# Kernel optimization log

Hardware: AMD Instinct MI355X
Metric: run time of the kernel (lower is better)

Reference implementation:

```python
import jax, jax.numpy as jnp
import numpy as np

N, IN_DIM, HID, H1, NCLS, H2, E = 50000, 256, 32, 8, 16, 8, 800000


def gat_conv(x, edge_index, W, a_src, a_dst, b, H, C):
    """PyG-style GATConv, eval mode (attention dropout off), concat=True,
    negative_slope=0.2, add_self_loops=True."""
    n = x.shape[0]
    loop = jnp.arange(n)
    src = jnp.concatenate([edge_index[0], loop])  # [E+N]
    dst = jnp.concatenate([edge_index[1], loop])
    h = (x @ W).reshape(n, H, C)                  # [N,H,C]
    alpha_s = jnp.sum(h * a_src, axis=-1)         # [N,H]
    alpha_d = jnp.sum(h * a_dst, axis=-1)         # [N,H]
    e = jax.nn.leaky_relu(alpha_s[src] + alpha_d[dst], 0.2)  # [E+N,H]
    # segment softmax over incoming edges of each target node
    e_max = jax.ops.segment_max(e, dst, num_segments=n)      # [N,H] (self-loop guarantees nonempty)
    p = jnp.exp(e - e_max[dst])
    denom = jax.ops.segment_sum(p, dst, num_segments=n)
    alpha = p / (denom[dst] + 1e-16)              # [E+N,H]
    msg = h[src] * alpha[:, :, None]              # [E+N,H,C]
    out = jax.ops.segment_sum(msg, dst, num_segments=n)      # [N,H,C]
    return out.reshape(n, H * C) + b


def setup_inputs() -> dict:
    key = jax.random.key(0)
    ks = jax.random.split(key, 12)
    x = jax.random.normal(ks[0], (N, IN_DIM), dtype=jnp.float32)
    edge_index = jax.random.randint(ks[1], (2, E), 0, N, dtype=jnp.int64)
    s1 = 1.0 / np.sqrt(IN_DIM)
    s2 = 1.0 / np.sqrt(HID * H1)
    W1 = jax.random.normal(ks[2], (IN_DIM, H1 * HID), dtype=jnp.float32) * s1
    a_src1 = jax.random.normal(ks[3], (H1, HID), dtype=jnp.float32) * s1
    a_dst1 = jax.random.normal(ks[4], (H1, HID), dtype=jnp.float32) * s1
    b1 = jnp.zeros((H1 * HID,), dtype=jnp.float32)
    W2 = jax.random.normal(ks[5], (H1 * HID, H2 * NCLS), dtype=jnp.float32) * s2
    a_src2 = jax.random.normal(ks[6], (H2, NCLS), dtype=jnp.float32) * s2
    a_dst2 = jax.random.normal(ks[7], (H2, NCLS), dtype=jnp.float32) * s2
    b2 = jnp.zeros((H2 * NCLS,), dtype=jnp.float32)
    return {"x": x, "edge_index": edge_index, "W1": W1, "a_src1": a_src1,
            "a_dst1": a_dst1, "b1": b1, "W2": W2, "a_src2": a_src2,
            "a_dst2": a_dst2, "b2": b2}


def reference(x, edge_index, W1, a_src1, a_dst1, b1, W2, a_src2, a_dst2, b2):
    # eval mode: F.dropout is identity
    h = gat_conv(x, edge_index, W1, a_src1, a_dst1, b1, H1, HID)   # [N, H1*HID]
    h = jax.nn.elu(h)
    h = gat_conv(h, edge_index, W2, a_src2, a_dst2, b2, H2, NCLS)  # [N, H2*NCLS]
    return jax.nn.log_softmax(h, axis=1)
```

## Files before the change

### kernel.cpp

```cpp
#include <hip/hip_runtime.h>
#include <hip/hip_fp16.h>

#define NN 50000
#define NE 800000

typedef _Float16 half4v __attribute__((ext_vector_type(4)));
typedef _Float16 half8v __attribute__((ext_vector_type(8)));
typedef float f32x4 __attribute__((ext_vector_type(4)));

#define Q_SCALE 0.04724409448f
#define Q_INV   21.16666667f

static __device__ __forceinline__ float lrelu(float x) { return x > 0.f ? x : 0.2f * x; }

__global__ void detect_i64_kernel(const unsigned* __restrict__ ei, int* __restrict__ flag) {
  if (threadIdx.x == 0 && blockIdx.x == 0) {
    int is64 = 1;
    for (int i = 0; i < 64; ++i)
      if (ei[2 * i + 1] != 0u) { is64 = 0; break; }
    *flag = is64;
  }
}

static __device__ __forceinline__ int edge_at(const void* ei, int is64, long long idx) {
  if (is64) return (int)((const long long*)ei)[idx];
  return ((const int*)ei)[idx];
}

__global__ void count_kernel(const void* __restrict__ ei, const int* __restrict__ flag,
                             int* __restrict__ counts) {
  int e = blockIdx.x * blockDim.x + threadIdx.x;
  if (e >= NE) return;
  int is64 = *flag;
  int d = edge_at(ei, is64, (long long)NE + e);
  atomicAdd(&counts[d], 1);
}

static __device__ __forceinline__ int block_scan_inc(int v, int tid) {
  __shared__ int ws[4];
  const int lane = tid & 63, wv = tid >> 6;
  #pragma unroll
  for (int off = 1; off < 64; off <<= 1) {
    int t = __shfl_up(v, off);
    if (lane >= off) v += t;
  }
  if (lane == 63) ws[wv] = v;
  __syncthreads();
  int add = 0;
  #pragma unroll
  for (int j = 0; j < 4; ++j) if (j < wv) add += ws[j];
  return v + add;
}

__global__ void scan1_kernel(const int* __restrict__ counts, int* __restrict__ bsums) {
  __shared__ int ws[4];
  const int tid = threadIdx.x;
  const int lane = tid & 63, wv = tid >> 6;
  int i = blockIdx.x * 256 + tid;
  int v = (i < NN) ? counts[i] : 0;
  #pragma unroll
  for (int off = 1; off < 64; off <<= 1) v += __shfl_xor(v, off);
  if (lane == 0) ws[wv] = v;
  __syncthreads();
  if (tid == 0) bsums[blockIdx.x] = ws[0] + ws[1] + ws[2] + ws[3];
}

__global__ void scan2_kernel(int* __restrict__ bsums, int nb) {
  const int tid = threadIdx.x;
  int v = (tid < nb) ? bsums[tid] : 0;
  int inc = block_scan_inc(v, tid);
  if (tid < nb) bsums[tid] = inc - v;
}

__global__ void scan3_kernel(const int* __restrict__ counts, const int* __restrict__ bsums,
                             int* __restrict__ rs) {
  const int tid = threadIdx.x;
  int i = blockIdx.x * 256 + tid;
  int v = (i < NN) ? counts[i] : 0;
  int inc = block_scan_inc(v, tid);
  if (i < NN) rs[i + 1] = bsums[blockIdx.x] + inc;
  if (i == 0) rs[0] = 0;
}

__global__ void scatter_kernel(const void* __restrict__ ei, const int* __restrict__ flag,
                               const int* __restrict__ rs, int* __restrict__ cursor,
                               int* __restrict__ ssrc) {
  int e = blockIdx.x * blockDim.x + threadIdx.x;
  if (e >= NE) return;
  int is64 = *flag;
  int s = edge_at(ei, is64, e);
  int d = edge_at(ei, is64, (long long)NE + e);
  int p = atomicAdd(&cursor[d], 1);
  ssrc[rs[d] + p] = s;
}

__global__ void prep_kernel(const float* __restrict__ W1, const float* __restrict__ W2,
                            const float* __restrict__ aS1, const float* __restrict__ aD1,
                            const float* __restrict__ aS2, const float* __restrict__ aD2,
                            _Float16* __restrict__ W1p, _Float16* __restrict__ W2p,
                            _Float16* __restrict__ Wa1p, _Float16* __restrict__ Wa2p) {
  int i = blockIdx.x * blockDim.x + threadIdx.x;
  if (i < 65536) {
    int j = i & 7, l = (i >> 3) & 63, kst = (i >> 9) & 7, ct = i >> 12;
    int col = ct * 16 + (l & 15);
    int k = kst * 32 + ((l >> 4) << 3) + j;
    W1p[i] = (_Float16)W1[(size_t)k * 256 + col];
  } else if (i < 98304) {
    int n = i - 65536;
    int j = n & 7, l = (n >> 3) & 63, kst = (n >> 9) & 7, ct = n >> 12;
    int col = ct * 16 + (l & 15);
    int k = kst * 32 + ((l >> 4) << 3) + j;
    W2p[n] = (_Float16)W2[(size_t)k * 128 + col];
  } else if (i < 102400) {
    int n = i - 98304;
    int j = n & 7, l = (n >> 3) & 63, kst = n >> 9;
    int row = l & 15;
    int head = row & 7;
    const float* a = (row < 8) ? aS1 : aD1;
    int k = kst * 32 + ((l >> 4) << 3) + j;
    float s = 0.f;
    #pragma unroll 8
    for (int c = 0; c < 32; ++c)
      s += W1[(size_t)k * 256 + head * 32 + c] * a[head * 32 + c];
    Wa1p[n] = (_Float16)s;
  } else if (i < 106496) {
    int n = i - 102400;
    int j = n & 7, l = (n >> 3) & 63, kst = n >> 9;
    int row = l & 15;
    int head = row & 7;
    const float* a = (row < 8) ? aS2 : aD2;
    int k = kst * 32 + ((l >> 4) << 3) + j;
    float s = 0.f;
    #pragma unroll 8
    for (int c = 0; c < 16; ++c)
      s += W2[(size_t)k * 128 + head * 16 + c] * a[head * 16 + c];
    Wa2p[n] = (_Float16)s;
  }
}

template<int BN, int NCF, bool A_HALF, bool Q8OUT>
__global__ __launch_bounds__(512) void gemm_mfma(const void* __restrict__ Araw,
                                                 const _Float16* __restrict__ Bp,
                                                 const _Float16* __restrict__ Wap,
                                                 void* __restrict__ Cout,
                                                 float* __restrict__ alS,
                                                 float* __restrict__ alD, int M) {
  __shared__ __align__(16) _Float16 As[64][256 + 8];
  const int tid = threadIdx.x;
  const int bm0 = blockIdx.x * 64;
  if (A_HALF) {
    const _Float16* A = (const _Float16*)Araw;
    half8v tmp[4]; int rr[4], cc[4];
    #pragma unroll
    for (int t = 0; t < 4; ++t) {
      int idx = tid + t * 512;
      int r = idx >> 5, c8 = (idx & 31) << 3;
      int gr = bm0 + r;
      tmp[t] = (half8v){};
      if (gr < M) tmp[t] = *(const half8v*)&A[(size_t)gr * 256 + c8];
      rr[t] = r; cc[t] = c8;
    }
    #pragma unroll
    for (int t = 0; t < 4; ++t)
      *(half8v*)&As[rr[t]][cc[t]] = tmp[t];
  } else {
    const float* A = (const float*)Araw;
    #pragma unroll
    for (int g = 0; g < 2; ++g) {
      float4 tmp[4]; int rr[4], cc[4];
      #pragma unroll
      for (int t = 0; t < 4; ++t) {
        int idx = tid + (g * 4 + t) * 512;
        int r = idx >> 6, c4 = (idx & 63) << 2;
        int gr = bm0 + r;
        tmp[t] = make_float4(0.f, 0.f, 0.f, 0.f);
        if (gr < M) tmp[t] = *(const float4*)&A[(size_t)gr * 256 + c4];
        rr[t] = r; cc[t] = c4;
      }
      #pragma unroll
      for (int t = 0; t < 4; ++t) {
        half4v h = { (_Float16)tmp[t].x, (_Float16)tmp[t].y,
                     (_Float16)tmp[t].z, (_Float16)tmp[t].w };
        *(half4v*)&As[rr[t]][cc[t]] = h;
      }
    }
  }
  __syncthreads();
  const int lane = tid & 63, wv = tid >> 6;
  const int ncol0 = wv * (16 * NCF);
  const int lrow = lane & 15, lk8 = (lane >> 4) << 3;
  f32x4 acc[4][NCF];
  f32x4 acca[4];
  #pragma unroll
  for (int rf = 0; rf < 4; ++rf) {
    acca[rf] = (f32x4){0.f, 0.f, 0.f, 0.f};
    #pragma unroll
    for (int cf = 0; cf < NCF; ++cf) acc[rf][cf] = (f32x4){0.f, 0.f, 0.f, 0.f};
  }
  #pragma unroll
  for (int kst = 0; kst < 8; ++kst) {
    const int ks = kst * 32 + lk8;
    half8v af[4];
    #pragma unroll
    for (int rf = 0; rf < 4; ++rf)
      af[rf] = *(const half8v*)&As[16 * rf + lrow][ks];
    #pragma unroll
    for (int cf = 0; cf < NCF; ++cf) {
      half8v bf = *(const half8v*)&Bp[((size_t)((wv * NCF + cf) * 8 + kst) * 64 + lane) * 8];
      #pragma unroll
      for (int rf = 0; rf < 4; ++rf)
        acc[rf][cf] = __builtin_amdgcn_mfma_f32_16x16x32_f16(af[rf], bf, acc[rf][cf], 0, 0, 0);
    }
    if (wv == 0) {
      half8v bfa = *(const half8v*)&Wap[((size_t)kst * 64 + lane) * 8];
      #pragma unroll
      for (int rf = 0; rf < 4; ++rf)
        acca[rf] = __builtin_amdgcn_mfma_f32_16x16x32_f16(af[rf], bfa, acca[rf], 0, 0, 0);
    }
  }
  if (Q8OUT) {
    __syncthreads();
    char* Cs = (char*)&As[0][0];
    #pragma unroll
    for (int rf = 0; rf < 4; ++rf) {
      #pragma unroll
      for (int j = 0; j < 4; ++j) {
        int r = 16 * rf + 4 * ((lane >> 4) & 3) + j;
        #pragma unroll
        for (int cf = 0; cf < NCF; ++cf) {
          int col = ncol0 + 16 * cf + lrow;
          float v = acc[rf][cf][j];
          int q = __float2int_rn(fminf(fmaxf(v * Q_INV, -127.f), 127.f)) + 128;
          Cs[r * 272 + col] = (char)q;
        }
      }
    }
    __syncthreads();
    unsigned char* C8 = (unsigned char*)Cout;
    #pragma unroll
    for (int g = 0; g < 2; ++g) {
      int idx = tid + g * 512;
      int r = idx >> 4, c16 = idx & 15;
      int grow = bm0 + r;
      if (grow < M)
        *(int4*)&C8[(size_t)grow * 256 + 16 * c16] = *(const int4*)&Cs[r * 272 + 16 * c16];
    }
  } else {
    __half* C = (__half*)Cout;
    #pragma unroll
    for (int rf = 0; rf < 4; ++rf) {
      #pragma unroll
      for (int j = 0; j < 4; ++j) {
        int row = bm0 + 16 * rf + 4 * ((lane >> 4) & 3) + j;
        if (row < M) {
          #pragma unroll
          for (int cf = 0; cf < NCF; ++cf) {
            int col = ncol0 + 16 * cf + lrow;
            C[(size_t)row * BN + col] = __float2half(acc[rf][cf][j]);
          }
        }
      }
    }
  }
  if (wv == 0) {
    #pragma unroll
    for (int rf = 0; rf < 4; ++rf) {
      #pragma unroll
      for (int j = 0; j < 4; ++j) {
        int row = bm0 + 16 * rf + 4 * ((lane >> 4) & 3) + j;
        if (row < M) {
          float v = acca[rf][j];
          if (lrow < 8) alS[row * 8 + lrow] = v;
          else          alD[row * 8 + (lrow - 8)] = v;
        }
      }
    }
  }
}

#define ACCQ(w, p) do { \
    ax0 += (p) * (float)((w) & 255u); \
    ax1 += (p) * (float)(((w) >> 8) & 255u); \
    ax2 += (p) * (float)(((w) >> 16) & 255u); \
    ax3 += (p) * (float)((w) >> 24); \
  } while (0)

__global__ __launch_bounds__(256) void agg1_kernel(const unsigned char* __restrict__ h1q,
    const float* __restrict__ as, const float* __restrict__ ad,
    const int* __restrict__ rs, const int* __restrict__ ssrc,
    const float* __restrict__ bias, __half* __restrict__ out) {
  const int wid = (blockIdx.x * blockDim.x + threadIdx.x) >> 6;
  const int lane = threadIdx.x & 63;
  if (wid >= NN) return;
  const int node = wid;
  const int beg = rs[node], end = rs[node + 1];
  const int deg = end - beg;
  const int hd = lane >> 3;
  const float advh = ad[node * 8 + hd];
  const unsigned* hw = (const unsigned*)h1q;
  float denom = 0.f;
  float ax0 = 0.f, ax1 = 0.f, ax2 = 0.f, ax3 = 0.f;
  {
    float p = __expf(lrelu(as[node * 8 + hd] + advh));
    unsigned w = hw[(size_t)node * 64 + lane];
    ACCQ(w, p);
    denom = p;
  }
  for (int base = 0; base < deg; base += 64) {
    const int cnt = min(deg - base, 64);
    int sv = (lane < cnt) ? ssrc[beg + base + lane] : 0;
    int j = 0;
    for (; j + 8 <= cnt; j += 8) {
      int s0 = __builtin_amdgcn_readlane(sv, j + 0);
      int s1 = __builtin_amdgcn_readlane(sv, j + 1);
      int s2 = __builtin_amdgcn_readlane(sv, j + 2);
      int s3 = __builtin_amdgcn_readlane(sv, j + 3);
      int s4 = __builtin_amdgcn_readlane(sv, j + 4);
      int s5 = __builtin_amdgcn_readlane(sv, j + 5);
      int s6 = __builtin_amdgcn_readlane(sv, j + 6);
      int s7 = __builtin_amdgcn_readlane(sv, j + 7);
      float b0 = as[s0 * 8 + hd], b1 = as[s1 * 8 + hd];
      float b2 = as[s2 * 8 + hd], b3 = as[s3 * 8 + hd];
      float b4 = as[s4 * 8 + hd], b5 = as[s5 * 8 + hd];
      float b6 = as[s6 * 8 + hd], b7 = as[s7 * 8 + hd];
      unsigned w0 = hw[(size_t)s0 * 64 + lane];
      unsigned w1 = hw[(size_t)s1 * 64 + lane];
      unsigned w2 = hw[(size_t)s2 * 64 + lane];
      unsigned w3 = hw[(size_t)s3 * 64 + lane];
      unsigned w4 = hw[(size_t)s4 * 64 + lane];
      unsigned w5 = hw[(size_t)s5 * 64 + lane];
      unsigned w6 = hw[(size_t)s6 * 64 + lane];
      unsigned w7 = hw[(size_t)s7 * 64 + lane];
      float p0 = __expf(lrelu(b0 + advh)), p1 = __expf(lrelu(b1 + advh));
      float p2 = __expf(lrelu(b2 + advh)), p3 = __expf(lrelu(b3 + advh));
      float p4 = __expf(lrelu(b4 + advh)), p5 = __expf(lrelu(b5 + advh));
      float p6 = __expf(lrelu(b6 + advh)), p7 = __expf(lrelu(b7 + advh));
      denom += (p0 + p1) + (p2 + p3) + ((p4 + p5) + (p6 + p7));
      ACCQ(w0, p0); ACCQ(w1, p1); ACCQ(w2, p2); ACCQ(w3, p3);
      ACCQ(w4, p4); ACCQ(w5, p5); ACCQ(w6, p6); ACCQ(w7, p7);
    }
    for (; j < cnt; ++j) {
      int s = __builtin_amdgcn_readlane(sv, j);
      float p = __expf(lrelu(as[s * 8 + hd] + advh));
      unsigned w = hw[(size_t)s * 64 + lane];
      ACCQ(w, p);
      denom += p;
    }
  }
  const float inv = 1.f / (denom + 1e-16f);
  const float4 bv = *(const float4*)&bias[lane * 4];
  float4 o;
  o.x = Q_SCALE * (ax0 * inv - 128.f) + bv.x;
  o.y = Q_SCALE * (ax1 * inv - 128.f) + bv.y;
  o.z = Q_SCALE * (ax2 * inv - 128.f) + bv.z;
  o.w = Q_SCALE * (ax3 * inv - 128.f) + bv.w;
  o.x = o.x > 0.f ? o.x : __expf(o.x) - 1.f;
  o.y = o.y > 0.f ? o.y : __expf(o.y) - 1.f;
  o.z = o.z > 0.f ? o.z : __expf(o.z) - 1.f;
  o.w = o.w > 0.f ? o.w : __expf(o.w) - 1.f;
  union { __half2 h2[2]; float2 f2; } w;
  w.h2[0] = __floats2half2_rn(o.x, o.y);
  w.h2[1] = __floats2half2_rn(o.z, o.w);
  *(float2*)&out[(size_t)node * 256 + lane * 4] = w.f2;
}

__global__ __launch_bounds__(256) void agg2_kernel(const __half* __restrict__ h,
    const float* __restrict__ as, const float* __restrict__ ad,
    const int* __restrict__ rs, const int* __restrict__ ssrc,
    const float* __restrict__ bias, float* __restrict__ out) {
  const int wid = (blockIdx.x * blockDim.x + threadIdx.x) >> 6;
  const int lane = threadIdx.x & 63;
  if (wid >= NN) return;
  const int node = wid;
  const int beg = rs[node], end = rs[node + 1];
  const int deg = end - beg;
  const int hd = lane >> 3;
  const float advh = ad[node * 8 + hd];
  float denom;
  __half2 acc;
  {
    float p = __expf(lrelu(as[node * 8 + hd] + advh));
    __half2 q = ((const __half2*)&h[(size_t)node * 128])[lane];
    acc = __hmul2(__float2half2_rn(p), q);
    denom = p;
  }
  for (int base = 0; base < deg; base += 64) {
    const int cnt = min(deg - base, 64);
    int sv = (lane < cnt) ? ssrc[beg + base + lane] : 0;
    int j = 0;
    for (; j + 8 <= cnt; j += 8) {
      int s0 = __builtin_amdgcn_readlane(sv, j + 0);
      int s1 = __builtin_amdgcn_readlane(sv, j + 1);
      int s2 = __builtin_amdgcn_readlane(sv, j + 2);
      int s3 = __builtin_amdgcn_readlane(sv, j + 3);
      int s4 = __builtin_amdgcn_readlane(sv, j + 4);
      int s5 = __builtin_amdgcn_readlane(sv, j + 5);
      int s6 = __builtin_amdgcn_readlane(sv, j + 6);
      int s7 = __builtin_amdgcn_readlane(sv, j + 7);
      float b0 = as[s0 * 8 + hd], b1 = as[s1 * 8 + hd];
      float b2 = as[s2 * 8 + hd], b3 = as[s3 * 8 + hd];
      float b4 = as[s4 * 8 + hd], b5 = as[s5 * 8 + hd];
      float b6 = as[s6 * 8 + hd], b7 = as[s7 * 8 + hd];
      __half2 q0 = ((const __half2*)&h[(size_t)s0 * 128])[lane];
      __half2 q1 = ((const __half2*)&h[(size_t)s1 * 128])[lane];
      __half2 q2 = ((const __half2*)&h[(size_t)s2 * 128])[lane];
      __half2 q3 = ((const __half2*)&h[(size_t)s3 * 128])[lane];
      __half2 q4 = ((const __half2*)&h[(size_t)s4 * 128])[lane];
      __half2 q5 = ((const __half2*)&h[(size_t)s5 * 128])[lane];
      __half2 q6 = ((const __half2*)&h[(size_t)s6 * 128])[lane];
      __half2 q7 = ((const __half2*)&h[(size_t)s7 * 128])[lane];
      float p0 = __expf(lrelu(b0 + advh)), p1 = __expf(lrelu(b1 + advh));
      float p2 = __expf(lrelu(b2 + advh)), p3 = __expf(lrelu(b3 + advh));
      float p4 = __expf(lrelu(b4 + advh)), p5 = __expf(lrelu(b5 + advh));
      float p6 = __expf(lrelu(b6 + advh)), p7 = __expf(lrelu(b7 + advh));
      denom += (p0 + p1) + (p2 + p3) + ((p4 + p5) + (p6 + p7));
      acc = __hfma2(__float2half2_rn(p0), q0, acc);
      acc = __hfma2(__float2half2_rn(p1), q1, acc);
      acc = __hfma2(__float2half2_rn(p2), q2, acc);
      acc = __hfma2(__float2half2_rn(p3), q3, acc);
      acc = __hfma2(__float2half2_rn(p4), q4, acc);
      acc = __hfma2(__float2half2_rn(p5), q5, acc);
      acc = __hfma2(__float2half2_rn(p6), q6, acc);
      acc = __hfma2(__float2half2_rn(p7), q7, acc);
    }
    for (; j < cnt; ++j) {
      int s = __builtin_amdgcn_readlane(sv, j);
      float p = __expf(lrelu(as[s * 8 + hd] + advh));
      __half2 q = ((const __half2*)&h[(size_t)s * 128])[lane];
      acc = __hfma2(__float2half2_rn(p), q, acc);
      denom += p;
    }
  }
  const float inv = 1.f / (denom + 1e-16f);
  float2 av = __half22float2(acc);
  float v0 = av.x * inv + bias[lane * 2 + 0];
  float v1 = av.y * inv + bias[lane * 2 + 1];
  float mx = fmaxf(v0, v1);
  #pragma unroll
  for (int off = 1; off < 64; off <<= 1) mx = fmaxf(mx, __shfl_xor(mx, off));
  float sum = __expf(v0 - mx) + __expf(v1 - mx);
  #pragma unroll
  for (int off = 1; off < 64; off <<= 1) sum += __shfl_xor(sum, off);
  float lse = mx + __logf(sum);
  float2 o = make_float2(v0 - lse, v1 - lse);
  __builtin_nontemporal_store(o.x, &out[(size_t)node * 128 + lane * 2]);
  __builtin_nontemporal_store(o.y, &out[(size_t)node * 128 + lane * 2 + 1]);
}

extern "C" void kernel_launch(void* const* d_in, const int* in_sizes, int n_in,
                              void* d_out, int out_size, void* d_ws, size_t ws_size,
                              hipStream_t stream) {
  const float* x    = (const float*)d_in[0];
  const void*  ei   = d_in[1];
  const float* W1   = (const float*)d_in[2];
  const float* aS1  = (const float*)d_in[3];
  const float* aD1  = (const float*)d_in[4];
  const float* b1   = (const float*)d_in[5];
  const float* W2   = (const float*)d_in[6];
  const float* aS2  = (const float*)d_in[7];
  const float* aD2  = (const float*)d_in[8];
  const float* b2   = (const float*)d_in[9];
  float* out = (float*)d_out;

  char* ws = (char*)d_ws;
  unsigned char* h1q = (unsigned char*)ws; ws += (size_t)NN * 256;
  __half* h2   = (__half*)ws;          ws += (size_t)NN * 128 * 2;
  __half* hmid = (__half*)ws;          ws += (size_t)NN * 256 * 2;
  _Float16* W1p = (_Float16*)ws;       ws += (size_t)65536 * 2;
  _Float16* W2p = (_Float16*)ws;       ws += (size_t)32768 * 2;
  _Float16* Wa1p = (_Float16*)ws;      ws += (size_t)4096 * 2;
  _Float16* Wa2p = (_Float16*)ws;      ws += (size_t)4096 * 2;
  float* alS  = (float*)ws;            ws += (size_t)NN * 8 * 4;
  float* alD  = (float*)ws;            ws += (size_t)NN * 8 * 4;
  int* counts = (int*)ws;              ws += (size_t)NN * 4;
  int* rs     = (int*)ws;              ws += (size_t)(NN + 1) * 4;
  int* bsums  = (int*)ws;              ws += (size_t)256 * 4;
  int* ssrc   = (int*)ws;              ws += (size_t)NE * 4;
  int* flag   = (int*)ws;              ws += 256;

  const int NB = (NN + 255) / 256;

  detect_i64_kernel<<<1, 64, 0, stream>>>((const unsigned*)ei, flag);
  hipMemsetAsync(counts, 0, (size_t)NN * 4, stream);
  count_kernel<<<(NE + 255) / 256, 256, 0, stream>>>(ei, flag, counts);
  scan1_kernel<<<NB, 256, 0, stream>>>(counts, bsums);
  scan2_kernel<<<1, 256, 0, stream>>>(bsums, NB);
  scan3_kernel<<<NB, 256, 0, stream>>>(counts, bsums, rs);
  hipMemsetAsync(counts, 0, (size_t)NN * 4, stream);
  scatter_kernel<<<(NE + 255) / 256, 256, 0, stream>>>(ei, flag, rs, counts, ssrc);

  prep_kernel<<<(106496 + 255) / 256, 256, 0, stream>>>(W1, W2, aS1, aD1, aS2, aD2,
                                                        W1p, W2p, Wa1p, Wa2p);

  const int ngrid = (NN + 63) / 64;
  gemm_mfma<256, 2, false, true><<<ngrid, 512, 0, stream>>>(x, W1p, Wa1p, h1q, alS, alD, NN);
  agg1_kernel<<<(NN + 3) / 4, 256, 0, stream>>>(h1q, alS, alD, rs, ssrc, b1, hmid);

  gemm_mfma<128, 1, true, false><<<ngrid, 512, 0, stream>>>(hmid, W2p, Wa2p, h2, alS, alD, NN);
  agg2_kernel<<<(NN + 3) / 4, 256, 0, stream>>>(h2, alS, alD, rs, ssrc, b2, out);
}
```

Measured before the change: 220.8 us.

## Quantize layer-2 features to uint8 and share attention exps via lane shuffles

The second GEMM now writes its projected features as 8-bit quantized bytes, using the same fixed scale as layer 1. agg2 gathers 2-byte words instead of half2 values and dequantizes into fp32 accumulators, which halves the gather traffic. Both aggregation kernels now compute each neighbor's attention exponent once per lane group and broadcast it with shuffles, instead of every lane loading alpha_src and computing exp. The cost is quantization error in the layer-2 features with a fixed scale that may clip, plus extra shuffle instructions.

```diff
diff --git a/kernel.cpp b/kernel.cpp
--- a/kernel.cpp
+++ b/kernel.cpp
@@ -220,6 +220,7 @@
   }
   if (Q8OUT) {
     __syncthreads();
+    constexpr int ROWB = BN + 16;
     char* Cs = (char*)&As[0][0];
     #pragma unroll
     for (int rf = 0; rf < 4; ++rf) {
@@ -231,19 +232,17 @@
           int col = ncol0 + 16 * cf + lrow;
           float v = acc[rf][cf][j];
           int q = __float2int_rn(fminf(fmaxf(v * Q_INV, -127.f), 127.f)) + 128;
-          Cs[r * 272 + col] = (char)q;
+          Cs[r * ROWB + col] = (char)q;
         }
       }
     }
     __syncthreads();
     unsigned char* C8 = (unsigned char*)Cout;
-    #pragma unroll
-    for (int g = 0; g < 2; ++g) {
-      int idx = tid + g * 512;
-      int r = idx >> 4, c16 = idx & 15;
+    for (int idx = tid; idx < 4 * BN; idx += 512) {
+      int r = idx / (BN / 16), c16 = idx % (BN / 16);
       int grow = bm0 + r;
       if (grow < M)
-        *(int4*)&C8[(size_t)grow * 256 + 16 * c16] = *(const int4*)&Cs[r * 272 + 16 * c16];
+        *(int4*)&C8[(size_t)grow * BN + 16 * c16] = *(const int4*)&Cs[r * ROWB + 16 * c16];
     }
   } else {
     __half* C = (__half*)Cout;
@@ -306,6 +305,7 @@
     ACCQ(w, p);
     denom = p;
   }
+  const int gb = lane & 56;
   for (int base = 0; base < deg; base += 64) {
     const int cnt = min(deg - base, 64);
     int sv = (lane < cnt) ? ssrc[beg + base + lane] : 0;
@@ -319,10 +319,6 @@
       int s5 = __builtin_amdgcn_readlane(sv, j + 5);
       int s6 = __builtin_amdgcn_readlane(sv, j + 6);
       int s7 = __builtin_amdgcn_readlane(sv, j + 7);
-      float b0 = as[s0 * 8 + hd], b1 = as[s1 * 8 + hd];
-      float b2 = as[s2 * 8 + hd], b3 = as[s3 * 8 + hd];
-      float b4 = as[s4 * 8 + hd], b5 = as[s5 * 8 + hd];
-      float b6 = as[s6 * 8 + hd], b7 = as[s7 * 8 + hd];
       unsigned w0 = hw[(size_t)s0 * 64 + lane];
       unsigned w1 = hw[(size_t)s1 * 64 + lane];
       unsigned w2 = hw[(size_t)s2 * 64 + lane];
@@ -331,10 +327,16 @@
       unsigned w5 = hw[(size_t)s5 * 64 + lane];
       unsigned w6 = hw[(size_t)s6 * 64 + lane];
       unsigned w7 = hw[(size_t)s7 * 64 + lane];
-      float p0 = __expf(lrelu(b0 + advh)), p1 = __expf(lrelu(b1 + advh));
-      float p2 = __expf(lrelu(b2 + advh)), p3 = __expf(lrelu(b3 + advh));
-      float p4 = __expf(lrelu(b4 + advh)), p5 = __expf(lrelu(b5 + advh));
-      float p6 = __expf(lrelu(b6 + advh)), p7 = __expf(lrelu(b7 + advh));
+      int sl = __shfl(sv, j + (lane & 7));
+      float pl = __expf(lrelu(as[(size_t)sl * 8 + hd] + advh));
+      float p0 = __shfl(pl, gb + 0);
+      float p1 = __shfl(pl, gb + 1);
+      float p2 = __shfl(pl, gb + 2);
+      float p3 = __shfl(pl, gb + 3);
+      float p4 = __shfl(pl, gb + 4);
+      float p5 = __shfl(pl, gb + 5);
+      float p6 = __shfl(pl, gb + 6);
+      float p7 = __shfl(pl, gb + 7);
       denom += (p0 + p1) + (p2 + p3) + ((p4 + p5) + (p6 + p7));
       ACCQ(w0, p0); ACCQ(w1, p1); ACCQ(w2, p2); ACCQ(w3, p3);
       ACCQ(w4, p4); ACCQ(w5, p5); ACCQ(w6, p6); ACCQ(w7, p7);
@@ -364,7 +366,12 @@
   *(float2*)&out[(size_t)node * 256 + lane * 4] = w.f2;
 }
 
-__global__ __launch_bounds__(256) void agg2_kernel(const __half* __restrict__ h,
+#define ACC2Q(w, p) do { \
+    ax0 += (p) * (float)((w) & 255u); \
+    ax1 += (p) * (float)(((w) >> 8) & 255u); \
+  } while (0)
+
+__global__ __launch_bounds__(256) void agg2_kernel(const unsigned char* __restrict__ h2q,
     const float* __restrict__ as, const float* __restrict__ ad,
     const int* __restrict__ rs, const int* __restrict__ ssrc,
     const float* __restrict__ bias, float* __restrict__ out) {
@@ -376,14 +383,16 @@
   const int deg = end - beg;
   const int hd = lane >> 3;
   const float advh = ad[node * 8 + hd];
-  float denom;
-  __half2 acc;
+  const unsigned short* hw = (const unsigned short*)h2q;
+  float denom = 0.f;
+  float ax0 = 0.f, ax1 = 0.f;
   {
     float p = __expf(lrelu(as[node * 8 + hd] + advh));
-    __half2 q = ((const __half2*)&h[(size_t)node * 128])[lane];
-    acc = __hmul2(__float2half2_rn(p), q);
+    unsigned w = hw[(size_t)node * 64 + lane];
+    ACC2Q(w, p);
     denom = p;
   }
+  const int gb = lane & 56;
   for (int base = 0; base < deg; base += 64) {
     const int cnt = min(deg - base, 64);
     int sv = (lane < cnt) ? ssrc[beg + base + lane] : 0;
@@ -397,44 +406,39 @@
       int s5 = __builtin_amdgcn_readlane(sv, j + 5);
       int s6 = __builtin_amdgcn_readlane(sv, j + 6);
       int s7 = __builtin_amdgcn_readlane(sv, j + 7);
-      float b0 = as[s0 * 8 + hd], b1 = as[s1 * 8 + hd];
-      float b2 = as[s2 * 8 + hd], b3 = as[s3 * 8 + hd];
-      float b4 = as[s4 * 8 + hd], b5 = as[s5 * 8 + hd];
-      float b6 = as[s6 * 8 + hd], b7 = as[s7 * 8 + hd];
-      __half2 q0 = ((const __half2*)&h[(size_t)s0 * 128])[lane];
-      __half2 q1 = ((const __half2*)&h[(size_t)s1 * 128])[lane];
-      __half2 q2 = ((const __half2*)&h[(size_t)s2 * 128])[lane];
-      __half2 q3 = ((const __half2*)&h[(size_t)s3 * 128])[lane];
-      __half2 q4 = ((const __half2*)&h[(size_t)s4 * 128])[lane];
-      __half2 q5 = ((const __half2*)&h[(size_t)s5 * 128])[lane];
-      __half2 q6 = ((const __half2*)&h[(size_t)s6 * 128])[lane];
-      __half2 q7 = ((const __half2*)&h[(size_t)s7 * 128])[lane];
-      float p0 = __expf(lrelu(b0 + advh)), p1 = __expf(lrelu(b1 + advh));
-      float p2 = __expf(lrelu(b2 + advh)), p3 = __expf(lrelu(b3 + advh));
-      float p4 = __expf(lrelu(b4 + advh)), p5 = __expf(lrelu(b5 + advh));
-      float p6 = __expf(lrelu(b6 + advh)), p7 = __expf(lrelu(b7 + advh));
+      unsigned w0 = hw[(size_t)s0 * 64 + lane];
+      unsigned w1 = hw[(size_t)s1 * 64 + lane];
+      unsigned w2 = hw[(size_t)s2 * 64 + lane];
+      unsigned w3 = hw[(size_t)s3 * 64 + lane];
+      unsigned w4 = hw[(size_t)s4 * 64 + lane];
+      unsigned w5 = hw[(size_t)s5 * 64 + lane];
+      unsigned w6 = hw[(size_t)s6 * 64 + lane];
+      unsigned w7 = hw[(size_t)s7 * 64 + lane];
+      int sl = __shfl(sv, j + (lane & 7));
+      float pl = __expf(lrelu(as[(size_t)sl * 8 + hd] + advh));
+      float p0 = __shfl(pl, gb + 0);
+      float p1 = __shfl(pl, gb + 1);
+      float p2 = __shfl(pl, gb + 2);
+      float p3 = __shfl(pl, gb + 3);
+      float p4 = __shfl(pl, gb + 4);
+      float p5 = __shfl(pl, gb + 5);
+      float p6 = __shfl(pl, gb + 6);
+      float p7 = __shfl(pl, gb + 7);
       denom += (p0 + p1) + (p2 + p3) + ((p4 + p5) + (p6 + p7));
-      acc = __hfma2(__float2half2_rn(p0), q0, acc);
-      acc = __hfma2(__float2half2_rn(p1), q1, acc);
-      acc = __hfma2(__float2half2_rn(p2), q2, acc);
-      acc = __hfma2(__float2half2_rn(p3), q3, acc);
-      acc = __hfma2(__float2half2_rn(p4), q4, acc);
-      acc = __hfma2(__float2half2_rn(p5), q5, acc);
-      acc = __hfma2(__float2half2_rn(p6), q6, acc);
-      acc = __hfma2(__float2half2_rn(p7), q7, acc);
+      ACC2Q(w0, p0); ACC2Q(w1, p1); ACC2Q(w2, p2); ACC2Q(w3, p3);
+      ACC2Q(w4, p4); ACC2Q(w5, p5); ACC2Q(w6, p6); ACC2Q(w7, p7);
     }
     for (; j < cnt; ++j) {
       int s = __builtin_amdgcn_readlane(sv, j);
       float p = __expf(lrelu(as[s * 8 + hd] + advh));
-      __half2 q = ((const __half2*)&h[(size_t)s * 128])[lane];
-      acc = __hfma2(__float2half2_rn(p), q, acc);
+      unsigned w = hw[(size_t)s * 64 + lane];
+      ACC2Q(w, p);
       denom += p;
     }
   }
   const float inv = 1.f / (denom + 1e-16f);
-  float2 av = __half22float2(acc);
-  float v0 = av.x * inv + bias[lane * 2 + 0];
-  float v1 = av.y * inv + bias[lane * 2 + 1];
+  float v0 = Q_SCALE * (ax0 * inv - 128.f) + bias[lane * 2 + 0];
+  float v1 = Q_SCALE * (ax1 * inv - 128.f) + bias[lane * 2 + 1];
   float mx = fmaxf(v0, v1);
   #pragma unroll
   for (int off = 1; off < 64; off <<= 1) mx = fmaxf(mx, __shfl_xor(mx, off));
@@ -464,7 +468,7 @@
 
   char* ws = (char*)d_ws;
   unsigned char* h1q = (unsigned char*)ws; ws += (size_t)NN * 256;
-  __half* h2   = (__half*)ws;          ws += (size_t)NN * 128 * 2;
+  unsigned char* h2q = (unsigned char*)ws; ws += (size_t)NN * 128;
   __half* hmid = (__half*)ws;          ws += (size_t)NN * 256 * 2;
   _Float16* W1p = (_Float16*)ws;       ws += (size_t)65536 * 2;
   _Float16* W2p = (_Float16*)ws;       ws += (size_t)32768 * 2;
@@ -496,6 +500,6 @@
   gemm_mfma<256, 2, false, true><<<ngrid, 512, 0, stream>>>(x, W1p, Wa1p, h1q, alS, alD, NN);
   agg1_kernel<<<(NN + 3) / 4, 256, 0, stream>>>(h1q, alS, alD, rs, ssrc, b1, hmid);
 
-  gemm_mfma<128, 1, true, false><<<ngrid, 512, 0, stream>>>(hmid, W2p, Wa2p, h2, alS, alD, NN);
-  agg2_kernel<<<(NN + 3) / 4, 256, 0, stream>>>(h2, alS, alD, rs, ssrc, b2, out);
-}
+  gemm_mfma<128, 1, true, true><<<ngrid, 512, 0, stream>>>(hmid, W2p, Wa2p, h2q, alS, alD, NN);
+  agg2_kernel<<<(NN + 3) / 4, 256, 0, stream>>>(h2q, alS, alD, rs, ssrc, b2, out);
+}
```

Result: no change. 222.8 us (+0.9%).
